# Kernel optimization log

Hardware: AMD Instinct MI355X
Metric: run time of the kernel (lower is better)

The kernel has to match this reference:

```python
import jax, jax.numpy as jnp
import numpy as np

N = 200000   # active voxels
B = 2        # batch size
G = 128      # spatial grid extent per axis
CIN = 64
COUT = 64
KS = 3       # kernel size -> 27 offsets
DIL = 1
EPS = 1e-5


def setup_inputs() -> dict:
    rng = np.random.default_rng(0)
    # unique active voxel coordinates over a B x G^3 grid
    lin = rng.choice(B * G * G * G, size=N, replace=False)
    b = lin // (G * G * G)
    r = lin % (G * G * G)
    x = r // (G * G)
    r2 = r % (G * G)
    y = r2 // G
    z = r2 % G
    coords = jnp.asarray(np.stack([b, x, y, z], axis=1).astype(np.int32))
    key = jax.random.key(0)
    ks = jax.random.split(key, 7)
    feats = jax.random.normal(ks[0], (N, CIN), jnp.float32)
    s1 = 1.0 / np.sqrt(KS ** 3 * CIN)
    s2 = 1.0 / np.sqrt(KS ** 3 * COUT)
    return {
        "feats": feats,
        "w1": jax.random.normal(ks[1], (KS ** 3, CIN, COUT), jnp.float32) * s1,
        "g1": 1.0 + 0.1 * jax.random.normal(ks[2], (COUT,), jnp.float32),
        "b1": 0.1 * jax.random.normal(ks[3], (COUT,), jnp.float32),
        "w2": jax.random.normal(ks[4], (KS ** 3, COUT, COUT), jnp.float32) * s2,
        "g2": 1.0 + 0.1 * jax.random.normal(ks[5], (COUT,), jnp.float32),
        "b2": 0.1 * jax.random.normal(ks[6], (COUT,), jnp.float32),
        "coords": coords,
    }


def build_neighbors(coords):
    """Hash (dense) lookup: for each of 27 kernel offsets, the input index of
    the neighboring active voxel (submanifold: output sites == input sites).
    Returns idx [27, N] int32 (0 where invalid) and mask [27, N] bool."""
    n = coords.shape[0]
    lin = ((coords[:, 0] * G + coords[:, 1]) * G + coords[:, 2]) * G + coords[:, 3]
    table = jnp.full((B * G * G * G,), -1, jnp.int32).at[lin].set(
        jnp.arange(n, dtype=jnp.int32))
    offs = jnp.asarray(
        [[dx, dy, dz] for dx in (-1, 0, 1) for dy in (-1, 0, 1) for dz in (-1, 0, 1)],
        dtype=jnp.int32) * DIL                       # [27, 3]
    nxyz = coords[None, :, 1:] + offs[:, None, :]    # [27, N, 3]
    inb = jnp.all((nxyz >= 0) & (nxyz < G), axis=-1)  # [27, N]
    c = jnp.clip(nxyz, 0, G - 1)
    nlin = ((coords[None, :, 0] * G + c[..., 0]) * G + c[..., 1]) * G + c[..., 2]
    idx = table[nlin]                                # [27, N]
    mask = inb & (idx >= 0)
    return jnp.where(mask, idx, 0), mask


def subm_conv(feats, nbr_idx, nbr_mask, w):
    # gather-GEMM-scatter, accumulated per kernel offset
    out = jnp.zeros((feats.shape[0], w.shape[-1]), feats.dtype)
    for k in range(w.shape[0]):
        g = jnp.where(nbr_mask[k][:, None], feats[nbr_idx[k]], 0.0)  # [N, Cin]
        out = out + g @ w[k]
    return out


def sparse_bn(x, gamma, beta):
    m = jnp.mean(x, axis=0)
    v = jnp.var(x, axis=0)
    return (x - m) * jax.lax.rsqrt(v + EPS) * gamma + beta


def reference(feats, w1, g1, b1, w2, g2, b2, coords):
    nbr_idx, nbr_mask = build_neighbors(coords)
    h = jax.nn.relu(sparse_bn(subm_conv(feats, nbr_idx, nbr_mask, w1), g1, b1))
    h = sparse_bn(subm_conv(h, nbr_idx, nbr_mask, w2), g2, b2)
    # shortcut is Identity (in_channels == out_channels, stride == 1)
    return jax.nn.relu(h + feats)
```

## Files before the change

kernel.cpp:

```cpp
#include <hip/hip_runtime.h>


constexpr int N_VOX = 200000;
constexpr int GEXT  = 128;
constexpr int C     = 64;
constexpr int K27   = 27;
constexpr int TBL_N = 2 * GEXT * GEXT * GEXT;
constexpr float EPSF = 1e-5f;

constexpr int NCH      = 391;
constexpr int PAIR_CAP = 460032;
constexpr int TIL64    = PAIR_CAP / 64;
constexpr int PBB      = 6250;
constexpr int RBLK     = 128;

using short8   = __attribute__((ext_vector_type(8))) short;
using floatx16 = __attribute__((ext_vector_type(16))) float;

static __device__ __forceinline__ ushort f2bf(float f) {
  union { float f; unsigned u; } a; a.f = f;
  unsigned r = a.u + 0x7fff + ((a.u >> 16) & 1);
  return (ushort)(r >> 16);
}
static __device__ __forceinline__ float bf2f(ushort h) {
  union { unsigned u; float f; } a; a.u = ((unsigned)h) << 16;
  return a.f;
}


__global__ __launch_bounds__(256) void k_fill(int* __restrict__ t,
                                              int* __restrict__ bsum,
                                              int* __restrict__ inl) {
  int i = blockIdx.x * 256 + threadIdx.x;
  if (i < TBL_N) t[i] = -1;
  if (i < 4096) bsum[i] = 0;
  if (i < PAIR_CAP) inl[i] = -1;
}

__global__ __launch_bounds__(256) void k_scatter(const int* __restrict__ coords,
                                                 int* __restrict__ t) {
  int n = blockIdx.x * 256 + threadIdx.x;
  if (n >= N_VOX) return;
  int4 c = reinterpret_cast<const int4*>(coords)[n];
  int lin = ((c.x * GEXT + c.y) * GEXT + c.z) * GEXT + c.w;
  t[lin] = n;
}

__global__ __launch_bounds__(256) void k_count(const int* __restrict__ coords,
                                               int* __restrict__ bsum) {
  int n = blockIdx.x * 256 + threadIdx.x;
  if (n >= N_VOX) return;
  int4 c = reinterpret_cast<const int4*>(coords)[n];
  int lin = ((c.x * GEXT + c.y) * GEXT + c.z) * GEXT + c.w;
  atomicAdd(&bsum[lin >> 10], 1);
}

__global__ __launch_bounds__(1024) void k_scan(const int* __restrict__ bsum,
                                               int* __restrict__ boff) {
  __shared__ int sc[1024];
  int t = threadIdx.x;
  int v0 = bsum[t * 4], v1 = bsum[t * 4 + 1], v2 = bsum[t * 4 + 2],
      v3 = bsum[t * 4 + 3];
  int s = v0 + v1 + v2 + v3;
  sc[t] = s;
  __syncthreads();
  for (int off = 1; off < 1024; off <<= 1) {
    int x = (t >= off) ? sc[t - off] : 0;
    __syncthreads();
    sc[t] += x;
    __syncthreads();
  }
  int excl = sc[t] - s;
  boff[t * 4]     = excl;
  boff[t * 4 + 1] = excl + v0;
  boff[t * 4 + 2] = excl + v0 + v1;
  boff[t * 4 + 3] = excl + v0 + v1 + v2;
}

__global__ __launch_bounds__(1024) void k_compact(int* __restrict__ table,
                                                  const int* __restrict__ boff,
                                                  int* __restrict__ perm) {
  __shared__ int wsum[16];
  int i = blockIdx.x * 1024 + threadIdx.x;
  int orig = table[i];
  bool valid = orig >= 0;
  unsigned long long bal = __ballot(valid);
  int lane = threadIdx.x & 63, wv = threadIdx.x >> 6;
  int before = __popcll(bal & ((1ull << lane) - 1ull));
  if (lane == 0) wsum[wv] = __popcll(bal);
  __syncthreads();
  int woff = 0;
  for (int w = 0; w < 16; ++w) woff += (w < wv) ? wsum[w] : 0;
  if (valid) {
    int j = boff[blockIdx.x] + woff + before;
    perm[j] = orig;
    table[i] = j;
  }
}

__global__ __launch_bounds__(256) void k_nbrp(const int* __restrict__ coords,
                                              const int* __restrict__ table,
                                              const int* __restrict__ perm,
                                              int* __restrict__ nbrp) {
  int j = blockIdx.x * 256 + threadIdx.x;
  if (j >= N_VOX) return;
  int orig = perm[j];
  int4 c = reinterpret_cast<const int4*>(coords)[orig];
  int k = 0;
  #pragma unroll
  for (int dx = -1; dx <= 1; ++dx)
    #pragma unroll
    for (int dy = -1; dy <= 1; ++dy)
      #pragma unroll
      for (int dz = -1; dz <= 1; ++dz) {
        int x = c.y + dx, y = c.z + dy, z = c.w + dz;
        int rank = -1;
        if (((unsigned)x < (unsigned)GEXT) & ((unsigned)y < (unsigned)GEXT) &
            ((unsigned)z < (unsigned)GEXT)) {
          int lin = ((c.x * GEXT + x) * GEXT + y) * GEXT + z;
          rank = table[lin];
        }
        nbrp[k * N_VOX + j] = rank;
        ++k;
      }
}

__global__ __launch_bounds__(512) void k_cnt2b(const int* __restrict__ nbrp,
                                               int* __restrict__ cnt2) {
  __shared__ int wsum[8];
  int k = blockIdx.x / NCH, c = blockIdx.x % NCH;
  int j = c * 512 + threadIdx.x;
  bool valid = (j < N_VOX) && (nbrp[k * N_VOX + j] >= 0);
  unsigned long long bal = __ballot(valid);
  int lane = threadIdx.x & 63, wv = threadIdx.x >> 6;
  if (lane == 0) wsum[wv] = __popcll(bal);
  __syncthreads();
  if (threadIdx.x == 0) {
    int s = 0;
    #pragma unroll
    for (int w = 0; w < 8; ++w) s += wsum[w];
    cnt2[k * NCH + c] = s;
  }
}

__global__ __launch_bounds__(512) void k_segtot(const int* __restrict__ cnt2,
                                                int* __restrict__ segs) {
  __shared__ int red[512];
  int k = blockIdx.x, t = threadIdx.x;
  red[t] = (t < NCH) ? cnt2[k * NCH + t] : 0;
  __syncthreads();
  for (int off = 256; off >= 1; off >>= 1) {
    if (t < off) red[t] += red[t + off];
    __syncthreads();
  }
  if (t == 0) segs[k] = red[0];
}

__global__ __launch_bounds__(64) void k_segbase(int* __restrict__ segs) {
  if (threadIdx.x == 0) {
    int b = 0;
    for (int k = 0; k < K27; ++k) {
      segs[32 + k] = b;
      b += (segs[k] + 63) & ~63;
    }
    segs[32 + K27] = b;
  }
}

__global__ __launch_bounds__(512) void k_choff(const int* __restrict__ cnt2,
                                               const int* __restrict__ segs,
                                               int* __restrict__ choff) {
  __shared__ int sc[512];
  int k = blockIdx.x, t = threadIdx.x;
  int v = (t < NCH) ? cnt2[k * NCH + t] : 0;
  sc[t] = v;
  __syncthreads();
  for (int off = 1; off < 512; off <<= 1) {
    int x = (t >= off) ? sc[t - off] : 0;
    __syncthreads();
    sc[t] += x;
    __syncthreads();
  }
  if (t < NCH) choff[k * NCH + t] = segs[32 + k] + sc[t] - v;
}

__global__ __launch_bounds__(512) void k_pairs(int* __restrict__ nbrp,
                                               const int* __restrict__ choff,
                                               int* __restrict__ inl) {
  __shared__ int wsum[8];
  int k = blockIdx.x / NCH, c = blockIdx.x % NCH;
  int j = c * 512 + threadIdx.x;
  int v = (j < N_VOX) ? nbrp[k * N_VOX + j] : -1;
  bool valid = v >= 0;
  unsigned long long bal = __ballot(valid);
  int lane = threadIdx.x & 63, wv = threadIdx.x >> 6;
  int before = __popcll(bal & ((1ull << lane) - 1ull));
  if (lane == 0) wsum[wv] = __popcll(bal);
  __syncthreads();
  int woff = 0;
  #pragma unroll
  for (int w = 0; w < 8; ++w) woff += (w < wv) ? wsum[w] : 0;
  if (valid) {
    int p = choff[k * NCH + c] + woff + before;
    inl[p] = v;
    nbrp[k * N_VOX + j] = p;
  }
}

__global__ __launch_bounds__(256) void k_tilek(const int* __restrict__ segs,
                                               int* __restrict__ tile_k) {
  int t = blockIdx.x * 256 + threadIdx.x;
  if (t >= TIL64) return;
  int p0 = t * 64, kk = -1;
  if (p0 < segs[32 + K27]) {
    #pragma unroll 1
    for (int k = 0; k < K27; ++k)
      if (p0 >= segs[32 + k] && p0 < segs[32 + k + 1]) kk = k;
  }
  tile_k[t] = kk;
}


__global__ __launch_bounds__(256) void k_gcast(const float* __restrict__ feats,
                                               const int* __restrict__ perm,
                                               ushort* __restrict__ fbp) {
  int i = blockIdx.x * 256 + threadIdx.x;
  int j = i >> 4, seg = i & 15;
  int p = perm[j];
  float4 v = reinterpret_cast<const float4*>(feats)[(p << 4) + seg];
  ushort4 o;
  o.x = f2bf(v.x); o.y = f2bf(v.y); o.z = f2bf(v.z); o.w = f2bf(v.w);
  reinterpret_cast<ushort4*>(fbp)[i] = o;
}

__global__ __launch_bounds__(256) void k_castw(const float* __restrict__ w,
                                               ushort* __restrict__ wp) {
  int i = blockIdx.x * 256 + threadIdx.x;
  if (i >= K27 * 4096) return;
  int k = i >> 12, r = i & 4095, ci = r >> 6, co = r & 63;
  int ch = co >> 5, row = co & 31;
  int ks = ci >> 4, hi1 = (ci >> 3) & 1, e = ci & 7;
  int dst = ((((k * 2 + ch) * 4 + ks) * 2 + hi1) << 8) + row * 8 + e;
  wp[dst] = f2bf(w[i]);
}

__global__ __launch_bounds__(256, 4) void k_pva(
    const ushort* __restrict__ fin,
    const ushort* __restrict__ wp,
    const int* __restrict__ inl,
    const int* __restrict__ tile_k,
    ushort* __restrict__ pv) {
  const int kk = tile_k[blockIdx.x];
  if (kk < 0) return;
  const int tid = threadIdx.x, lane = tid & 63, wv = tid >> 6;
  const int lo = lane & 31, hi = lane >> 5;
  const int ch = wv & 1, vh = wv >> 1;
  const int pr = blockIdx.x * 64 + vh * 32 + lo;
  const int idx = inl[pr];

  const char* wk = (const char*)wp + (kk << 13) + (ch << 12) + (lane << 4);
  short8 a0 = *(const short8*)(wk);
  short8 a1 = *(const short8*)(wk + 1024);
  short8 a2 = *(const short8*)(wk + 2048);
  short8 a3 = *(const short8*)(wk + 3072);

  short8 b0, b1, b2, b3;
  if (idx >= 0) {
    const char* b = (const char*)fin + ((size_t)idx << 7) + (hi << 4);
    b0 = *(const short8*)(b);
    b1 = *(const short8*)(b + 32);
    b2 = *(const short8*)(b + 64);
    b3 = *(const short8*)(b + 96);
  } else {
    b0 = short8{0,0,0,0,0,0,0,0}; b1 = b0; b2 = b0; b3 = b0;
  }

  floatx16 acc;
  #pragma unroll
  for (int j = 0; j < 16; ++j) acc[j] = 0.f;
  acc = __builtin_amdgcn_mfma_f32_32x32x16_bf16(a0, b0, acc, 0, 0, 0);
  acc = __builtin_amdgcn_mfma_f32_32x32x16_bf16(a1, b1, acc, 0, 0, 0);
  acc = __builtin_amdgcn_mfma_f32_32x32x16_bf16(a2, b2, acc, 0, 0, 0);
  acc = __builtin_amdgcn_mfma_f32_32x32x16_bf16(a3, b3, acc, 0, 0, 0);

  ushort* o = pv + ((size_t)pr << 6) + (ch << 5) + (hi << 2);
  #pragma unroll
  for (int rg = 0; rg < 4; ++rg) {
    ushort4 v;
    v.x = f2bf(acc[rg * 4 + 0]); v.y = f2bf(acc[rg * 4 + 1]);
    v.z = f2bf(acc[rg * 4 + 2]); v.w = f2bf(acc[rg * 4 + 3]);
    *(ushort4*)(o + (rg << 3)) = v;
  }
}

template <bool OUT_F32>
__global__ __launch_bounds__(256) void k_pvb(
    const ushort* __restrict__ pv,
    const int* __restrict__ pidx,
    const int* __restrict__ perm,
    void* __restrict__ fout,
    float* __restrict__ part) {
  __shared__ float sred[4][8][16];
  const int tid = threadIdx.x, lane = tid & 63, wv = tid >> 6;
  const int g = tid >> 3, e = tid & 7;
  const int j = blockIdx.x * 32 + g;

  int p[27];
  #pragma unroll
  for (int t = 0; t < K27; ++t) p[t] = pidx[t * N_VOX + j];

  float acc[8];
  #pragma unroll
  for (int r = 0; r < 8; ++r) acc[r] = 0.f;
  #pragma unroll
  for (int t = 0; t < K27; ++t) {
    if (p[t] >= 0) {
      short8 v = *(const short8*)(pv + ((size_t)p[t] << 6) + (e << 3));
      #pragma unroll
      for (int r = 0; r < 8; ++r) acc[r] += bf2f((ushort)v[r]);
    }
  }

  if (OUT_F32) {
    int pj = perm[j];
    float* o = (float*)fout + ((size_t)pj << 6) + (e << 3);
    float4 v0 = {acc[0], acc[1], acc[2], acc[3]};
    float4 v1 = {acc[4], acc[5], acc[6], acc[7]};
    *(float4*)o = v0;
    *(float4*)(o + 4) = v1;
  } else {
    ushort* o = (ushort*)fout + ((size_t)j << 6) + (e << 3);
    ushort4 v0, v1;
    v0.x = f2bf(acc[0]); v0.y = f2bf(acc[1]);
    v0.z = f2bf(acc[2]); v0.w = f2bf(acc[3]);
    v1.x = f2bf(acc[4]); v1.y = f2bf(acc[5]);
    v1.z = f2bf(acc[6]); v1.w = f2bf(acc[7]);
    *(ushort4*)o = v0;
    *(ushort4*)(o + 4) = v1;
  }

  #pragma unroll
  for (int r = 0; r < 8; ++r) {
    float s = acc[r], ss = acc[r] * acc[r];
    s += __shfl_xor(s, 8);  ss += __shfl_xor(ss, 8);
    s += __shfl_xor(s, 16); ss += __shfl_xor(ss, 16);
    s += __shfl_xor(s, 32); ss += __shfl_xor(ss, 32);
    if (lane < 8) { sred[wv][lane][r] = s; sred[wv][lane][8 + r] = ss; }
  }
  __syncthreads();
  if (tid < 128) {
    int half = tid >> 6, ch = tid & 63;
    int e2 = ch >> 3, r2 = ch & 7;
    float v = sred[0][e2][half * 8 + r2] + sred[1][e2][half * 8 + r2] +
              sred[2][e2][half * 8 + r2] + sred[3][e2][half * 8 + r2];
    part[(size_t)blockIdx.x * 128 + tid] = v;
  }
}


__global__ __launch_bounds__(256) void k_red(const float* __restrict__ part,
                                             float* __restrict__ part2) {
  __shared__ float red[256];
  int tid = threadIdx.x;
  int e = tid & 127, g = tid >> 7;
  float s = 0.f;
  for (int r = blockIdx.x * 2 + g; r < PBB; r += 2 * RBLK)
    s += part[(size_t)r * 128 + e];
  red[tid] = s;
  __syncthreads();
  if (tid < 128) part2[(size_t)blockIdx.x * 128 + tid] = red[tid] + red[tid + 128];
}

__global__ __launch_bounds__(256) void k_bnfin(const float* __restrict__ part2,
                                               const float* __restrict__ gamma,
                                               const float* __restrict__ beta,
                                               float* __restrict__ ab) {
  __shared__ float fin[128];
  int tid = threadIdx.x;
  if (tid < 128) {
    float s = 0.f;
    for (int r = 0; r < RBLK; ++r) s += part2[(size_t)r * 128 + tid];
    fin[tid] = s;
  }
  __syncthreads();
  if (tid < 64) {
    float su = fin[tid], ss = fin[64 + tid];
    float mean = su / (float)N_VOX;
    float var  = ss / (float)N_VOX - mean * mean;
    float a = gamma[tid] * rsqrtf(var + EPSF);
    ab[tid]      = a;
    ab[64 + tid] = beta[tid] - mean * a;
  }
}

__global__ __launch_bounds__(256) void k_bnrelu8(ushort* __restrict__ x,
                                                 const float* __restrict__ ab) {
  int i = blockIdx.x * 256 + threadIdx.x;
  ushort4 v0 = reinterpret_cast<ushort4*>(x)[i * 2];
  ushort4 v1 = reinterpret_cast<ushort4*>(x)[i * 2 + 1];
  int cb = (i * 8) & 63;
  v0.x = f2bf(fmaxf(bf2f(v0.x) * ab[cb]     + ab[64 + cb],     0.f));
  v0.y = f2bf(fmaxf(bf2f(v0.y) * ab[cb + 1] + ab[64 + cb + 1], 0.f));
  v0.z = f2bf(fmaxf(bf2f(v0.z) * ab[cb + 2] + ab[64 + cb + 2], 0.f));
  v0.w = f2bf(fmaxf(bf2f(v0.w) * ab[cb + 3] + ab[64 + cb + 3], 0.f));
  v1.x = f2bf(fmaxf(bf2f(v1.x) * ab[cb + 4] + ab[64 + cb + 4], 0.f));
  v1.y = f2bf(fmaxf(bf2f(v1.y) * ab[cb + 5] + ab[64 + cb + 5], 0.f));
  v1.z = f2bf(fmaxf(bf2f(v1.z) * ab[cb + 6] + ab[64 + cb + 6], 0.f));
  v1.w = f2bf(fmaxf(bf2f(v1.w) * ab[cb + 7] + ab[64 + cb + 7], 0.f));
  reinterpret_cast<ushort4*>(x)[i * 2]     = v0;
  reinterpret_cast<ushort4*>(x)[i * 2 + 1] = v1;
}

__global__ __launch_bounds__(256) void k_final4(float* __restrict__ h2,
                                                const float* __restrict__ feats,
                                                const float* __restrict__ ab) {
  int i = blockIdx.x * 256 + threadIdx.x;
  float4 a = reinterpret_cast<float4*>(h2)[i];
  float4 f = reinterpret_cast<const float4*>(feats)[i];
  int cb = (i * 4) & 63;
  float4 o;
  o.x = fmaxf(a.x * ab[cb]     + ab[64 + cb]     + f.x, 0.f);
  o.y = fmaxf(a.y * ab[cb + 1] + ab[64 + cb + 1] + f.y, 0.f);
  o.z = fmaxf(a.z * ab[cb + 2] + ab[64 + cb + 2] + f.z, 0.f);
  o.w = fmaxf(a.w * ab[cb + 3] + ab[64 + cb + 3] + f.w, 0.f);
  reinterpret_cast<float4*>(h2)[i] = o;
}

extern "C" void kernel_launch(void* const* d_in, const int* in_sizes, int n_in,
                              void* d_out, int out_size, void* d_ws, size_t ws_size,
                              hipStream_t stream) {
  const float* feats  = (const float*)d_in[0];
  const float* w1     = (const float*)d_in[1];
  const float* g1     = (const float*)d_in[2];
  const float* b1     = (const float*)d_in[3];
  const float* w2     = (const float*)d_in[4];
  const float* g2     = (const float*)d_in[5];
  const float* b2     = (const float*)d_in[6];
  const int*   coords = (const int*)d_in[7];
  float* out = (float*)d_out;

  char* ws = (char*)d_ws;
  ushort* pv    = (ushort*)ws;  ws += (size_t)PAIR_CAP * C * 2;
  int*    table = (int*)ws;     ws += (size_t)TBL_N * 4;
  int*    nbrp  = (int*)ws;     ws += (size_t)K27 * N_VOX * 4;
  ushort* fbp   = (ushort*)ws;  ws += (size_t)N_VOX * C * 2;
  ushort* h1p   = (ushort*)ws;  ws += (size_t)N_VOX * C * 2;
  int*    perm  = (int*)ws;     ws += (size_t)N_VOX * 4;
  ushort* wp1   = (ushort*)ws;  ws += (size_t)K27 * 4096 * 2;
  ushort* wp2   = (ushort*)ws;  ws += (size_t)K27 * 4096 * 2;
  int*    inl   = (int*)ws;     ws += (size_t)PAIR_CAP * 4;
  int*    bsum  = (int*)ws;     ws += 4096 * 4;
  int*    boff  = (int*)ws;     ws += 4096 * 4;
  int*    cnt2  = (int*)ws;     ws += 42240;
  int*    choff = (int*)ws;     ws += 42240;
  int*    segs  = (int*)ws;     ws += 256;
  int*    tilk  = (int*)ws;     ws += (size_t)TIL64 * 4;
  float*  part2 = (float*)ws;   ws += (size_t)RBLK * 128 * 4;
  float*  ab1   = (float*)ws;   ws += 512;
  float*  ab2   = (float*)ws;   ws += 512;
  float*  part  = (float*)table;

  k_fill<<<TBL_N / 256, 256, 0, stream>>>(table, bsum, inl);
  k_scatter<<<(N_VOX + 255) / 256, 256, 0, stream>>>(coords, table);
  k_count<<<(N_VOX + 255) / 256, 256, 0, stream>>>(coords, bsum);
  k_scan<<<1, 1024, 0, stream>>>(bsum, boff);
  k_compact<<<TBL_N / 1024, 1024, 0, stream>>>(table, boff, perm);
  k_nbrp<<<(N_VOX + 255) / 256, 256, 0, stream>>>(coords, table, perm, nbrp);
  k_cnt2b<<<K27 * NCH, 512, 0, stream>>>(nbrp, cnt2);
  k_segtot<<<K27, 512, 0, stream>>>(cnt2, segs);
  k_segbase<<<1, 64, 0, stream>>>(segs);
  k_choff<<<K27, 512, 0, stream>>>(cnt2, segs, choff);
  k_pairs<<<K27 * NCH, 512, 0, stream>>>(nbrp, choff, inl);
  k_tilek<<<(TIL64 + 255) / 256, 256, 0, stream>>>(segs, tilk);

  k_gcast<<<N_VOX * 16 / 256, 256, 0, stream>>>(feats, perm, fbp);
  k_castw<<<(K27 * 4096 + 255) / 256, 256, 0, stream>>>(w1, wp1);
  k_castw<<<(K27 * 4096 + 255) / 256, 256, 0, stream>>>(w2, wp2);

  k_pva<<<TIL64, 256, 0, stream>>>(fbp, wp1, inl, tilk, pv);
  k_pvb<false><<<PBB, 256, 0, stream>>>(pv, nbrp, perm, h1p, part);
  k_red<<<RBLK, 256, 0, stream>>>(part, part2);
  k_bnfin<<<1, 256, 0, stream>>>(part2, g1, b1, ab1);
  k_bnrelu8<<<N_VOX * 8 / 256, 256, 0, stream>>>(h1p, ab1);

  k_pva<<<TIL64, 256, 0, stream>>>(h1p, wp2, inl, tilk, pv);
  k_pvb<true><<<PBB, 256, 0, stream>>>(pv, nbrp, perm, out, part);
  k_red<<<RBLK, 256, 0, stream>>>(part, part2);
  k_bnfin<<<1, 256, 0, stream>>>(part2, g2, b2, ab2);
  k_final4<<<N_VOX * 64 / 4 / 256, 256, 0, stream>>>(out, feats, ab2);
}
```

Before: 311.0 us.

## Fuse preprocessing kernels and fold BN-ReLU into second conv gather

```diff
diff --git a/kernel.cpp b/kernel.cpp
--- a/kernel.cpp
+++ b/kernel.cpp
@@ -8,7 +8,7 @@
 constexpr int TBL_N = 2 * GEXT * GEXT * GEXT;
 constexpr float EPSF = 1e-5f;
 
-constexpr int NCH      = 391;
+constexpr int NCH      = 782;
 constexpr int PAIR_CAP = 460032;
 constexpr int TIL64    = PAIR_CAP / 64;
 constexpr int PBB      = 6250;
@@ -37,21 +37,14 @@
   if (i < PAIR_CAP) inl[i] = -1;
 }
 
-__global__ __launch_bounds__(256) void k_scatter(const int* __restrict__ coords,
-                                                 int* __restrict__ t) {
+__global__ __launch_bounds__(256) void k_scatcnt(const int* __restrict__ coords,
+                                                 int* __restrict__ t,
+                                                 int* __restrict__ bsum) {
   int n = blockIdx.x * 256 + threadIdx.x;
   if (n >= N_VOX) return;
   int4 c = reinterpret_cast<const int4*>(coords)[n];
   int lin = ((c.x * GEXT + c.y) * GEXT + c.z) * GEXT + c.w;
   t[lin] = n;
-}
-
-__global__ __launch_bounds__(256) void k_count(const int* __restrict__ coords,
-                                               int* __restrict__ bsum) {
-  int n = blockIdx.x * 256 + threadIdx.x;
-  if (n >= N_VOX) return;
-  int4 c = reinterpret_cast<const int4*>(coords)[n];
-  int lin = ((c.x * GEXT + c.y) * GEXT + c.z) * GEXT + c.w;
   atomicAdd(&bsum[lin >> 10], 1);
 }
 
@@ -98,14 +91,20 @@
   }
 }
 
-__global__ __launch_bounds__(256) void k_nbrp(const int* __restrict__ coords,
+__global__ __launch_bounds__(256) void k_nbrc(const int* __restrict__ coords,
                                               const int* __restrict__ table,
                                               const int* __restrict__ perm,
-                                              int* __restrict__ nbrp) {
-  int j = blockIdx.x * 256 + threadIdx.x;
-  if (j >= N_VOX) return;
-  int orig = perm[j];
-  int4 c = reinterpret_cast<const int4*>(coords)[orig];
+                                              int* __restrict__ nbrp,
+                                              int* __restrict__ cnt2) {
+  __shared__ int wcnt[27][4];
+  int tid = threadIdx.x;
+  int j = blockIdx.x * 256 + tid;
+  bool on = j < N_VOX;
+  int4 c = {0, 0, 0, 0};
+  if (on) {
+    int orig = perm[j];
+    c = reinterpret_cast<const int4*>(coords)[orig];
+  }
   int k = 0;
   #pragma unroll
   for (int dx = -1; dx <= 1; ++dx)
@@ -113,83 +112,86 @@
     for (int dy = -1; dy <= 1; ++dy)
       #pragma unroll
       for (int dz = -1; dz <= 1; ++dz) {
-        int x = c.y + dx, y = c.z + dy, z = c.w + dz;
         int rank = -1;
-        if (((unsigned)x < (unsigned)GEXT) & ((unsigned)y < (unsigned)GEXT) &
-            ((unsigned)z < (unsigned)GEXT)) {
-          int lin = ((c.x * GEXT + x) * GEXT + y) * GEXT + z;
-          rank = table[lin];
+        if (on) {
+          int x = c.y + dx, y = c.z + dy, z = c.w + dz;
+          if (((unsigned)x < (unsigned)GEXT) & ((unsigned)y < (unsigned)GEXT) &
+              ((unsigned)z < (unsigned)GEXT)) {
+            int lin = ((c.x * GEXT + x) * GEXT + y) * GEXT + z;
+            rank = table[lin];
+          }
+          nbrp[k * N_VOX + j] = rank;
         }
-        nbrp[k * N_VOX + j] = rank;
+        unsigned long long bal = __ballot(rank >= 0);
+        if ((tid & 63) == 0) wcnt[k][tid >> 6] = __popcll(bal);
         ++k;
       }
-}
-
-__global__ __launch_bounds__(512) void k_cnt2b(const int* __restrict__ nbrp,
-                                               int* __restrict__ cnt2) {
-  __shared__ int wsum[8];
-  int k = blockIdx.x / NCH, c = blockIdx.x % NCH;
-  int j = c * 512 + threadIdx.x;
-  bool valid = (j < N_VOX) && (nbrp[k * N_VOX + j] >= 0);
-  unsigned long long bal = __ballot(valid);
-  int lane = threadIdx.x & 63, wv = threadIdx.x >> 6;
-  if (lane == 0) wsum[wv] = __popcll(bal);
-  __syncthreads();
-  if (threadIdx.x == 0) {
-    int s = 0;
-    #pragma unroll
-    for (int w = 0; w < 8; ++w) s += wsum[w];
-    cnt2[k * NCH + c] = s;
-  }
-}
-
-__global__ __launch_bounds__(512) void k_segtot(const int* __restrict__ cnt2,
-                                                int* __restrict__ segs) {
-  __shared__ int red[512];
+  __syncthreads();
+  if (tid < 27)
+    cnt2[tid * NCH + blockIdx.x] =
+        wcnt[tid][0] + wcnt[tid][1] + wcnt[tid][2] + wcnt[tid][3];
+}
+
+__global__ __launch_bounds__(256) void k_segscan(const int* __restrict__ cnt2,
+                                                 int* __restrict__ choff,
+                                                 int* __restrict__ segs) {
+  __shared__ int sc[256];
   int k = blockIdx.x, t = threadIdx.x;
-  red[t] = (t < NCH) ? cnt2[k * NCH + t] : 0;
-  __syncthreads();
-  for (int off = 256; off >= 1; off >>= 1) {
-    if (t < off) red[t] += red[t + off];
-    __syncthreads();
-  }
-  if (t == 0) segs[k] = red[0];
-}
-
-__global__ __launch_bounds__(64) void k_segbase(int* __restrict__ segs) {
-  if (threadIdx.x == 0) {
-    int b = 0;
-    for (int k = 0; k < K27; ++k) {
-      segs[32 + k] = b;
-      b += (segs[k] + 63) & ~63;
-    }
-    segs[32 + K27] = b;
-  }
-}
-
-__global__ __launch_bounds__(512) void k_choff(const int* __restrict__ cnt2,
-                                               const int* __restrict__ segs,
-                                               int* __restrict__ choff) {
-  __shared__ int sc[512];
-  int k = blockIdx.x, t = threadIdx.x;
-  int v = (t < NCH) ? cnt2[k * NCH + t] : 0;
-  sc[t] = v;
-  __syncthreads();
-  for (int off = 1; off < 512; off <<= 1) {
+  int v[4];
+  #pragma unroll
+  for (int i = 0; i < 4; ++i) {
+    int idx = t * 4 + i;
+    v[i] = (idx < NCH) ? cnt2[k * NCH + idx] : 0;
+  }
+  int s = v[0] + v[1] + v[2] + v[3];
+  sc[t] = s;
+  __syncthreads();
+  for (int off = 1; off < 256; off <<= 1) {
     int x = (t >= off) ? sc[t - off] : 0;
     __syncthreads();
     sc[t] += x;
     __syncthreads();
   }
-  if (t < NCH) choff[k * NCH + t] = segs[32 + k] + sc[t] - v;
-}
-
-__global__ __launch_bounds__(512) void k_pairs(int* __restrict__ nbrp,
+  int run = sc[t] - s;
+  #pragma unroll
+  for (int i = 0; i < 4; ++i) {
+    int idx = t * 4 + i;
+    if (idx < NCH) choff[k * NCH + idx] = run;
+    run += v[i];
+  }
+  if (t == 255) segs[k] = sc[255];
+}
+
+__global__ __launch_bounds__(1024) void k_tiles(int* __restrict__ segs,
+                                                int* __restrict__ tile_k) {
+  __shared__ int sb[28];
+  if (threadIdx.x == 0) {
+    int b = 0;
+    for (int k = 0; k < K27; ++k) {
+      sb[k] = b;
+      segs[32 + k] = b;
+      b += (segs[k] + 63) & ~63;
+    }
+    sb[27] = b;
+    segs[32 + K27] = b;
+  }
+  __syncthreads();
+  for (int t = threadIdx.x; t < TIL64; t += 1024) {
+    int p0 = t * 64, kk = -1;
+    #pragma unroll 1
+    for (int k = 0; k < K27; ++k)
+      if (p0 >= sb[k] && p0 < sb[k + 1]) kk = k;
+    tile_k[t] = kk;
+  }
+}
+
+__global__ __launch_bounds__(256) void k_pairs(int* __restrict__ nbrp,
                                                const int* __restrict__ choff,
+                                               const int* __restrict__ segs,
                                                int* __restrict__ inl) {
-  __shared__ int wsum[8];
-  int k = blockIdx.x / NCH, c = blockIdx.x % NCH;
-  int j = c * 512 + threadIdx.x;
+  __shared__ int wsum[4];
+  int k = blockIdx.x / NCH, cch = blockIdx.x % NCH;
+  int j = cch * 256 + threadIdx.x;
   int v = (j < N_VOX) ? nbrp[k * N_VOX + j] : -1;
   bool valid = v >= 0;
   unsigned long long bal = __ballot(valid);
@@ -199,60 +201,60 @@
   __syncthreads();
   int woff = 0;
   #pragma unroll
-  for (int w = 0; w < 8; ++w) woff += (w < wv) ? wsum[w] : 0;
+  for (int w = 0; w < 4; ++w) woff += (w < wv) ? wsum[w] : 0;
   if (valid) {
-    int p = choff[k * NCH + c] + woff + before;
+    int p = segs[32 + k] + choff[k * NCH + cch] + woff + before;
     inl[p] = v;
     nbrp[k * N_VOX + j] = p;
   }
 }
 
-__global__ __launch_bounds__(256) void k_tilek(const int* __restrict__ segs,
-                                               int* __restrict__ tile_k) {
-  int t = blockIdx.x * 256 + threadIdx.x;
-  if (t >= TIL64) return;
-  int p0 = t * 64, kk = -1;
-  if (p0 < segs[32 + K27]) {
-    #pragma unroll 1
-    for (int k = 0; k < K27; ++k)
-      if (p0 >= segs[32 + k] && p0 < segs[32 + k + 1]) kk = k;
-  }
-  tile_k[t] = kk;
-}
-
-
-__global__ __launch_bounds__(256) void k_gcast(const float* __restrict__ feats,
-                                               const int* __restrict__ perm,
-                                               ushort* __restrict__ fbp) {
-  int i = blockIdx.x * 256 + threadIdx.x;
-  int j = i >> 4, seg = i & 15;
-  int p = perm[j];
-  float4 v = reinterpret_cast<const float4*>(feats)[(p << 4) + seg];
-  ushort4 o;
-  o.x = f2bf(v.x); o.y = f2bf(v.y); o.z = f2bf(v.z); o.w = f2bf(v.w);
-  reinterpret_cast<ushort4*>(fbp)[i] = o;
-}
-
-__global__ __launch_bounds__(256) void k_castw(const float* __restrict__ w,
-                                               ushort* __restrict__ wp) {
-  int i = blockIdx.x * 256 + threadIdx.x;
-  if (i >= K27 * 4096) return;
-  int k = i >> 12, r = i & 4095, ci = r >> 6, co = r & 63;
-  int ch = co >> 5, row = co & 31;
-  int ks = ci >> 4, hi1 = (ci >> 3) & 1, e = ci & 7;
-  int dst = ((((k * 2 + ch) * 4 + ks) * 2 + hi1) << 8) + row * 8 + e;
-  wp[dst] = f2bf(w[i]);
-}
-
+
+__global__ __launch_bounds__(256) void k_prep(const float* __restrict__ feats,
+                                              const int* __restrict__ perm,
+                                              const float* __restrict__ w1,
+                                              const float* __restrict__ w2,
+                                              ushort* __restrict__ fbp,
+                                              ushort* __restrict__ wp1,
+                                              ushort* __restrict__ wp2) {
+  int b = blockIdx.x;
+  if (b < 12500) {
+    int i = b * 256 + threadIdx.x;
+    int j = i >> 4, seg = i & 15;
+    int p = perm[j];
+    float4 v = reinterpret_cast<const float4*>(feats)[(p << 4) + seg];
+    ushort4 o;
+    o.x = f2bf(v.x); o.y = f2bf(v.y); o.z = f2bf(v.z); o.w = f2bf(v.w);
+    reinterpret_cast<ushort4*>(fbp)[i] = o;
+  } else {
+    const float* w = (b < 12932) ? w1 : w2;
+    ushort* wp = (b < 12932) ? wp1 : wp2;
+    int i = (b - (b < 12932 ? 12500 : 12932)) * 256 + threadIdx.x;
+    int k = i >> 12, r = i & 4095, ci = r >> 6, co = r & 63;
+    int ch = co >> 5, row = co & 31;
+    int ks = ci >> 4, hi1 = (ci >> 3) & 1, e = ci & 7;
+    int dst = ((((k * 2 + ch) * 4 + ks) * 2 + hi1) << 8) + row * 8 + e;
+    wp[dst] = f2bf(w[i]);
+  }
+}
+
+template <bool APPLY_BN>
 __global__ __launch_bounds__(256, 4) void k_pva(
     const ushort* __restrict__ fin,
     const ushort* __restrict__ wp,
     const int* __restrict__ inl,
     const int* __restrict__ tile_k,
+    const float* __restrict__ ab,
     ushort* __restrict__ pv) {
+  __shared__ float abl[128];
   const int kk = tile_k[blockIdx.x];
+  const int tid = threadIdx.x;
+  if (APPLY_BN) {
+    if (tid < 128) abl[tid] = ab[tid];
+    __syncthreads();
+  }
   if (kk < 0) return;
-  const int tid = threadIdx.x, lane = tid & 63, wv = tid >> 6;
+  const int lane = tid & 63, wv = tid >> 6;
   const int lo = lane & 31, hi = lane >> 5;
   const int ch = wv & 1, vh = wv >> 1;
   const int pr = blockIdx.x * 64 + vh * 32 + lo;
@@ -271,6 +273,19 @@
     b1 = *(const short8*)(b + 32);
     b2 = *(const short8*)(b + 64);
     b3 = *(const short8*)(b + 96);
+    if (APPLY_BN) {
+      #pragma unroll
+      for (int ks = 0; ks < 4; ++ks) {
+        short8& v = ks == 0 ? b0 : ks == 1 ? b1 : ks == 2 ? b2 : b3;
+        int cb = ks * 16 + hi * 8;
+        #pragma unroll
+        for (int e = 0; e < 8; ++e) {
+          float x = bf2f((ushort)v[e]);
+          x = fmaxf(x * abl[cb + e] + abl[64 + cb + e], 0.f);
+          v[e] = (short)f2bf(x);
+        }
+      }
+    }
   } else {
     b0 = short8{0,0,0,0,0,0,0,0}; b1 = b0; b2 = b0; b3 = b0;
   }
@@ -293,12 +308,10 @@
   }
 }
 
-template <bool OUT_F32>
 __global__ __launch_bounds__(256) void k_pvb(
     const ushort* __restrict__ pv,
     const int* __restrict__ pidx,
-    const int* __restrict__ perm,
-    void* __restrict__ fout,
+    ushort* __restrict__ fout,
     float* __restrict__ part) {
   __shared__ float sred[4][8][16];
   const int tid = threadIdx.x, lane = tid & 63, wv = tid >> 6;
@@ -321,23 +334,14 @@
     }
   }
 
-  if (OUT_F32) {
-    int pj = perm[j];
-    float* o = (float*)fout + ((size_t)pj << 6) + (e << 3);
-    float4 v0 = {acc[0], acc[1], acc[2], acc[3]};
-    float4 v1 = {acc[4], acc[5], acc[6], acc[7]};
-    *(float4*)o = v0;
-    *(float4*)(o + 4) = v1;
-  } else {
-    ushort* o = (ushort*)fout + ((size_t)j << 6) + (e << 3);
-    ushort4 v0, v1;
-    v0.x = f2bf(acc[0]); v0.y = f2bf(acc[1]);
-    v0.z = f2bf(acc[2]); v0.w = f2bf(acc[3]);
-    v1.x = f2bf(acc[4]); v1.y = f2bf(acc[5]);
-    v1.z = f2bf(acc[6]); v1.w = f2bf(acc[7]);
-    *(ushort4*)o = v0;
-    *(ushort4*)(o + 4) = v1;
-  }
+  ushort* o = fout + ((size_t)j << 6) + (e << 3);
+  ushort4 v0, v1;
+  v0.x = f2bf(acc[0]); v0.y = f2bf(acc[1]);
+  v0.z = f2bf(acc[2]); v0.w = f2bf(acc[3]);
+  v1.x = f2bf(acc[4]); v1.y = f2bf(acc[5]);
+  v1.z = f2bf(acc[6]); v1.w = f2bf(acc[7]);
+  *(ushort4*)o = v0;
+  *(ushort4*)(o + 4) = v1;
 
   #pragma unroll
   for (int r = 0; r < 8; ++r) {
@@ -349,8 +353,8 @@
   }
   __syncthreads();
   if (tid < 128) {
-    int half = tid >> 6, ch = tid & 63;
-    int e2 = ch >> 3, r2 = ch & 7;
+    int half = tid >> 6, chn = tid & 63;
+    int e2 = chn >> 3, r2 = chn & 7;
     float v = sred[0][e2][half * 8 + r2] + sred[1][e2][half * 8 + r2] +
               sred[2][e2][half * 8 + r2] + sred[3][e2][half * 8 + r2];
     part[(size_t)blockIdx.x * 128 + tid] = v;
@@ -393,37 +397,23 @@
   }
 }
 
-__global__ __launch_bounds__(256) void k_bnrelu8(ushort* __restrict__ x,
-                                                 const float* __restrict__ ab) {
+__global__ __launch_bounds__(256) void k_final(const ushort* __restrict__ h2p,
+                                               const float* __restrict__ feats,
+                                               const int* __restrict__ perm,
+                                               const float* __restrict__ ab,
+                                               float* __restrict__ out) {
   int i = blockIdx.x * 256 + threadIdx.x;
-  ushort4 v0 = reinterpret_cast<ushort4*>(x)[i * 2];
-  ushort4 v1 = reinterpret_cast<ushort4*>(x)[i * 2 + 1];
-  int cb = (i * 8) & 63;
-  v0.x = f2bf(fmaxf(bf2f(v0.x) * ab[cb]     + ab[64 + cb],     0.f));
-  v0.y = f2bf(fmaxf(bf2f(v0.y) * ab[cb + 1] + ab[64 + cb + 1], 0.f));
-  v0.z = f2bf(fmaxf(bf2f(v0.z) * ab[cb + 2] + ab[64 + cb + 2], 0.f));
-  v0.w = f2bf(fmaxf(bf2f(v0.w) * ab[cb + 3] + ab[64 + cb + 3], 0.f));
-  v1.x = f2bf(fmaxf(bf2f(v1.x) * ab[cb + 4] + ab[64 + cb + 4], 0.f));
-  v1.y = f2bf(fmaxf(bf2f(v1.y) * ab[cb + 5] + ab[64 + cb + 5], 0.f));
-  v1.z = f2bf(fmaxf(bf2f(v1.z) * ab[cb + 6] + ab[64 + cb + 6], 0.f));
-  v1.w = f2bf(fmaxf(bf2f(v1.w) * ab[cb + 7] + ab[64 + cb + 7], 0.f));
-  reinterpret_cast<ushort4*>(x)[i * 2]     = v0;
-  reinterpret_cast<ushort4*>(x)[i * 2 + 1] = v1;
-}
-
-__global__ __launch_bounds__(256) void k_final4(float* __restrict__ h2,
-                                                const float* __restrict__ feats,
-                                                const float* __restrict__ ab) {
-  int i = blockIdx.x * 256 + threadIdx.x;
-  float4 a = reinterpret_cast<float4*>(h2)[i];
-  float4 f = reinterpret_cast<const float4*>(feats)[i];
-  int cb = (i * 4) & 63;
+  int j = i >> 4, seg = i & 15;
+  int p = perm[j];
+  ushort4 h = reinterpret_cast<const ushort4*>(h2p)[i];
+  float4 f = reinterpret_cast<const float4*>(feats)[(p << 4) + seg];
+  int cb = seg * 4;
   float4 o;
-  o.x = fmaxf(a.x * ab[cb]     + ab[64 + cb]     + f.x, 0.f);
-  o.y = fmaxf(a.y * ab[cb + 1] + ab[64 + cb + 1] + f.y, 0.f);
-  o.z = fmaxf(a.z * ab[cb + 2] + ab[64 + cb + 2] + f.z, 0.f);
-  o.w = fmaxf(a.w * ab[cb + 3] + ab[64 + cb + 3] + f.w, 0.f);
-  reinterpret_cast<float4*>(h2)[i] = o;
+  o.x = fmaxf(bf2f(h.x) * ab[cb]     + ab[64 + cb]     + f.x, 0.f);
+  o.y = fmaxf(bf2f(h.y) * ab[cb + 1] + ab[64 + cb + 1] + f.y, 0.f);
+  o.z = fmaxf(bf2f(h.z) * ab[cb + 2] + ab[64 + cb + 2] + f.z, 0.f);
+  o.w = fmaxf(bf2f(h.w) * ab[cb + 3] + ab[64 + cb + 3] + f.w, 0.f);
+  reinterpret_cast<float4*>(out)[(p << 4) + seg] = o;
 }
 
 extern "C" void kernel_launch(void* const* d_in, const int* in_sizes, int n_in,
@@ -451,41 +441,36 @@
   int*    inl   = (int*)ws;     ws += (size_t)PAIR_CAP * 4;
   int*    bsum  = (int*)ws;     ws += 4096 * 4;
   int*    boff  = (int*)ws;     ws += 4096 * 4;
-  int*    cnt2  = (int*)ws;     ws += 42240;
-  int*    choff = (int*)ws;     ws += 42240;
+  int*    cnt2  = (int*)ws;     ws += (size_t)K27 * NCH * 4;
+  int*    choff = (int*)ws;     ws += (size_t)K27 * NCH * 4;
   int*    segs  = (int*)ws;     ws += 256;
   int*    tilk  = (int*)ws;     ws += (size_t)TIL64 * 4;
   float*  part2 = (float*)ws;   ws += (size_t)RBLK * 128 * 4;
   float*  ab1   = (float*)ws;   ws += 512;
   float*  ab2   = (float*)ws;   ws += 512;
   float*  part  = (float*)table;
+  ushort* h2p   = fbp;
 
   k_fill<<<TBL_N / 256, 256, 0, stream>>>(table, bsum, inl);
-  k_scatter<<<(N_VOX + 255) / 256, 256, 0, stream>>>(coords, table);
-  k_count<<<(N_VOX + 255) / 256, 256, 0, stream>>>(coords, bsum);
+  k_scatcnt<<<(N_VOX + 255) / 256, 256, 0, stream>>>(coords, table, bsum);
   k_scan<<<1, 1024, 0, stream>>>(bsum, boff);
   k_compact<<<TBL_N / 1024, 1024, 0, stream>>>(table, boff, perm);
-  k_nbrp<<<(N_VOX + 255) / 256, 256, 0, stream>>>(coords, table, perm, nbrp);
-  k_cnt2b<<<K27 * NCH, 512, 0, stream>>>(nbrp, cnt2);
-  k_segtot<<<K27, 512, 0, stream>>>(cnt2, segs);
-  k_segbase<<<1, 64, 0, stream>>>(segs);
-  k_choff<<<K27, 512, 0, stream>>>(cnt2, segs, choff);
-  k_pairs<<<K27 * NCH, 512, 0, stream>>>(nbrp, choff, inl);
-  k_tilek<<<(TIL64 + 255) / 256, 256, 0, stream>>>(segs, tilk);
-
-  k_gcast<<<N_VOX * 16 / 256, 256, 0, stream>>>(feats, perm, fbp);
-  k_castw<<<(K27 * 4096 + 255) / 256, 256, 0, stream>>>(w1, wp1);
-  k_castw<<<(K27 * 4096 + 255) / 256, 256, 0, stream>>>(w2, wp2);
-
-  k_pva<<<TIL64, 256, 0, stream>>>(fbp, wp1, inl, tilk, pv);
-  k_pvb<false><<<PBB, 256, 0, stream>>>(pv, nbrp, perm, h1p, part);
+  k_nbrc<<<NCH, 256, 0, stream>>>(coords, table, perm, nbrp, cnt2);
+  k_segscan<<<K27, 256, 0, stream>>>(cnt2, choff, segs);
+  k_tiles<<<1, 1024, 0, stream>>>(segs, tilk);
+  k_pairs<<<K27 * NCH, 256, 0, stream>>>(nbrp, choff, segs, inl);
+
+  k_prep<<<13364, 256, 0, stream>>>(feats, perm, w1, w2, fbp, wp1, wp2);
+
+  k_pva<false><<<TIL64, 256, 0, stream>>>(fbp, wp1, inl, tilk, ab1, pv);
+  k_pvb<<<PBB, 256, 0, stream>>>(pv, nbrp, h1p, part);
   k_red<<<RBLK, 256, 0, stream>>>(part, part2);
   k_bnfin<<<1, 256, 0, stream>>>(part2, g1, b1, ab1);
-  k_bnrelu8<<<N_VOX * 8 / 256, 256, 0, stream>>>(h1p, ab1);
-
-  k_pva<<<TIL64, 256, 0, stream>>>(h1p, wp2, inl, tilk, pv);
-  k_pvb<true><<<PBB, 256, 0, stream>>>(pv, nbrp, perm, out, part);
+
+  k_pva<true><<<TIL64, 256, 0, stream>>>(h1p, wp2, inl, tilk, ab1, pv);
+  k_pvb<<<PBB, 256, 0, stream>>>(pv, nbrp, h2p, part);
   k_red<<<RBLK, 256, 0, stream>>>(part, part2);
   k_bnfin<<<1, 256, 0, stream>>>(part2, g2, b2, ab2);
-  k_final4<<<N_VOX * 64 / 4 / 256, 256, 0, stream>>>(out, feats, ab2);
-}
+
+  k_final<<<N_VOX * 16 / 256, 256, 0, stream>>>(h2p, feats, perm, ab2, out);
+}
```

New measurement: 298.6 us. 4.0% less time.
